# Kernel tuning notes

Measured on AMD Instinct MI355X. Metric: run time of the kernel, lower is better.

Reference implementation:

```python
import jax, jax.numpy as jnp
import numpy as np

N_HEADS = 16


def setup_inputs() -> dict:
    key = jax.random.key(0)
    ks = jax.random.split(key, 9)
    B, S, D = 4, 2048, 1024
    query = jax.random.normal(ks[0], (B, S, D), dtype=jnp.float32)
    key_t = jax.random.normal(ks[1], (B, S, D), dtype=jnp.float32)
    value = jax.random.normal(ks[2], (B, S, D), dtype=jnp.float32)
    mask = jax.random.randint(ks[3], (B, 1, S, S), 0, 10) > 0
    scale_w = 0.02  # keep exp(attention) in a safe range
    Wq = jax.random.normal(ks[4], (D, D), dtype=jnp.float32) * scale_w
    Wk = jax.random.normal(ks[5], (D, D), dtype=jnp.float32) * scale_w
    Wv = jax.random.normal(ks[6], (D, D), dtype=jnp.float32) * scale_w
    fc_w = jax.random.normal(ks[7], (D, D), dtype=jnp.float32) * scale_w
    fc_b = jnp.zeros((D,), dtype=jnp.float32)
    return {"query": query, "key": key_t, "value": value, "mask": mask,
            "Wq": Wq, "Wk": Wk, "Wv": Wv, "fc_w": fc_w, "fc_b": fc_b}


def reference(query, key, value, mask, Wq, Wk, Wv, fc_w, fc_b):
    B, S, D = query.shape
    H = N_HEADS
    Dh = D // H
    scale = jnp.sqrt(jnp.asarray(D / H, dtype=query.dtype))
    # Faithful to original: direct reshape [B,S,D] -> [B,H,S,Dh] (no transpose)
    Q = (query @ Wq.T).reshape(B, H, S, Dh)
    K = (key @ Wk.T).reshape(B, H, S, Dh)
    V = (value @ Wv.T).reshape(B, H, S, Dh)
    attn = jnp.einsum('bhqd,bhkd->bhqk', Q, K) / scale  # [B,H,S,S]
    # Hand-rolled masked softmax: exp, masked_fill(False->0), normalize, nan->0
    temp = jnp.where(mask, jnp.exp(attn), 0.0)
    attn = temp / jnp.sum(temp, axis=-1, keepdims=True)
    attn = jnp.where(jnp.isnan(attn), 0.0, attn)
    res = jnp.einsum('bhqk,bhkd->bhqd', attn, V)  # [B,H,S,Dh]
    outs = res.transpose(0, 2, 1, 3).reshape(B, S, D)
    outs = outs @ fc_w.T + fc_b
    return outs, res.transpose(1, 0, 2, 3)
```

## Files before the change

kernel.cpp:

```cpp
#include <hip/hip_runtime.h>


typedef __attribute__((ext_vector_type(8))) short bf16x8;
typedef __attribute__((ext_vector_type(4))) short bf16x4;
typedef __attribute__((ext_vector_type(4))) float f32x4;

#define MFMA32(a, b, c) __builtin_amdgcn_mfma_f32_16x16x32_bf16(a, b, c, 0, 0, 0)

#define GLDS16(g, l)                                                                       \
  __builtin_amdgcn_global_load_lds((const __attribute__((address_space(1))) void*)(g),     \
                                   (__attribute__((address_space(3))) void*)(l), 16, 0, 0)

static __device__ __forceinline__ float fast_exp2(float x) {
#if __has_builtin(__builtin_amdgcn_exp2f)
  return __builtin_amdgcn_exp2f(x);
#else
  return __expf(x * 0.69314718056f);
#endif
}

__device__ __forceinline__ unsigned short fbf(float f) {
  union { float f; unsigned u; } x; x.f = f;
  unsigned r = x.u + 0x7fffu + ((x.u >> 16) & 1u);
  return (unsigned short)(r >> 16);
}

static __device__ __forceinline__ bf16x4 pack2(unsigned lo, unsigned hi) {
  union { unsigned u[2]; bf16x4 v; } x; x.u[0] = lo; x.u[1] = hi; return x.v;
}

static __device__ __forceinline__ bf16x8 cat2(bf16x4 lo, bf16x4 hi) {
  union { bf16x4 h[2]; bf16x8 v; } x; x.h[0] = lo; x.h[1] = hi; return x.v;
}

static __device__ __forceinline__ bf16x4 epp(f32x4 s, unsigned pre, int sh) {
  union { float f; unsigned u; } e0, e1, e2, e3;
  e0.f = fast_exp2(s[0]); e1.f = fast_exp2(s[1]);
  e2.f = fast_exp2(s[2]); e3.f = fast_exp2(s[3]);
  unsigned p01 = __builtin_amdgcn_perm(e1.u + 0x8000u, e0.u + 0x8000u, 0x07060302u);
  unsigned p23 = __builtin_amdgcn_perm(e3.u + 0x8000u, e2.u + 0x8000u, 0x07060302u);
  int m0 = __builtin_amdgcn_sbfe(pre, sh + 0, 1), m1 = __builtin_amdgcn_sbfe(pre, sh + 1, 1);
  int m2 = __builtin_amdgcn_sbfe(pre, sh + 2, 1), m3 = __builtin_amdgcn_sbfe(pre, sh + 3, 1);
  unsigned k01 = __builtin_amdgcn_perm((unsigned)m1, (unsigned)m0, 0x07060100u);
  unsigned k23 = __builtin_amdgcn_perm((unsigned)m3, (unsigned)m2, 0x07060100u);
  return pack2(p01 & k01, p23 & k23);
}

__global__ __launch_bounds__(256) void prep_kernel(const float* __restrict__ s0,
                                                   const float* __restrict__ s1,
                                                   const float* __restrict__ s2,
                                                   const float* __restrict__ w0,
                                                   const float* __restrict__ w1,
                                                   const float* __restrict__ w2,
                                                   const float* __restrict__ w3,
                                                   unsigned short* __restrict__ d0,
                                                   unsigned short* __restrict__ d1,
                                                   unsigned short* __restrict__ d2,
                                                   unsigned short* __restrict__ e0,
                                                   unsigned short* __restrict__ e1,
                                                   unsigned short* __restrict__ e2,
                                                   unsigned short* __restrict__ e3) {
  int bid = blockIdx.x;
  const float* s;
  unsigned short* d;
  int i;
  if (bid < 24576) {
    int z = bid >> 13;
    s = (z == 0) ? s0 : (z == 1) ? s1 : s2;
    d = (z == 0) ? d0 : (z == 1) ? d1 : d2;
    i = (bid & 8191) * 256 + threadIdx.x;
  } else {
    int r = bid - 24576;
    int z = r >> 10;
    s = (z == 0) ? w0 : (z == 1) ? w1 : (z == 2) ? w2 : w3;
    d = (z == 0) ? e0 : (z == 1) ? e1 : (z == 2) ? e2 : e3;
    i = (r & 1023) * 256 + threadIdx.x;
  }
  float4 v = ((const float4*)s)[i];
  ushort4 o;
  o.x = fbf(v.x); o.y = fbf(v.y); o.z = fbf(v.z); o.w = fbf(v.w);
  ((ushort4*)d)[i] = o;
}

__global__ __launch_bounds__(256) void pack_mask_kernel(const int* __restrict__ m,
                                                        unsigned long long* __restrict__ o) {
  int i = blockIdx.x * 256 + threadIdx.x;
  unsigned long long b = __ballot(m[i] != 0);
  if ((threadIdx.x & 63) == 0) {
    int row = i >> 11;
    int kt = (i >> 7) & 15;
    int h = (i >> 6) & 1;
    o[(kt * 8192 + row) * 2 + h] = b;
  }
}

__global__ __launch_bounds__(256) void vtrans_kernel(const unsigned short* __restrict__ Vf,
                                                     unsigned short* __restrict__ Vt) {
  __shared__ unsigned short T[64][72];
  const int bh = blockIdx.y;
  const int s0 = blockIdx.x * 64;
  const int tid = threadIdx.x;
  {
    int r = tid >> 2, c = (tid & 3) * 16;
    const unsigned short* src = Vf + bh * 131072 + (s0 + r) * 64 + c;
    uint4 v0 = *(const uint4*)(src);
    uint4 v1 = *(const uint4*)(src + 8);
    *(uint4*)&T[r][c] = v0;
    *(uint4*)&T[r][c + 8] = v1;
  }
  __syncthreads();
  {
    int dh = tid & 63, rb = (tid >> 6) * 16;
    unsigned short o[16];
#pragma unroll
    for (int j = 0; j < 16; ++j) o[j] = T[rb + j][dh];
    unsigned short* dst = Vt + bh * 131072 + dh * 2048 + s0 + rb;
    *(uint4*)dst = *(const uint4*)&o[0];
    *(uint4*)(dst + 8) = *(const uint4*)&o[8];
  }
}

__global__ __launch_bounds__(256) void proj_kernel(const unsigned short* __restrict__ A0,
                                                   const unsigned short* __restrict__ A1,
                                                   const unsigned short* __restrict__ A2,
                                                   const unsigned short* __restrict__ W0,
                                                   const unsigned short* __restrict__ W1,
                                                   const unsigned short* __restrict__ W2,
                                                   unsigned short* __restrict__ C0,
                                                   unsigned short* __restrict__ C1,
                                                   unsigned short* __restrict__ C2) {
  __shared__ unsigned short Alds[128 * 64];
  __shared__ unsigned short Blds[128 * 64];
  const int flat = (blockIdx.z * 64 + blockIdx.y) * 8 + blockIdx.x;
  const int wid = (flat & 7) * 192 + (flat >> 3);
  const int z = wid >> 9;
  const int by = (wid >> 3) & 63;
  const int bx = wid & 7;
  const unsigned short* A = (z == 0) ? A0 : (z == 1) ? A1 : A2;
  const unsigned short* B = (z == 0) ? W0 : (z == 1) ? W1 : W2;
  const int tid = threadIdx.x;
  const int w = tid >> 6, l = tid & 63, q4 = l >> 4, c16 = l & 15;
  const int wm = w & 1, wn = w >> 1;
  const int mBase = by * 128, nBase = bx * 128;

  f32x4 acc[4][4];
#pragma unroll
  for (int a0 = 0; a0 < 4; ++a0)
#pragma unroll
    for (int a1 = 0; a1 < 4; ++a1) acc[a0][a1] = (f32x4){0.f, 0.f, 0.f, 0.f};

  const int rsub = tid >> 3;
  const int csw = ((tid & 7) ^ (rsub & 7)) * 8;

  for (int kt = 0; kt < 16; ++kt) {
    __syncthreads();
#pragma unroll
    for (int j = 0; j < 4; ++j) {
      const unsigned short* gA = A + (mBase + j * 32 + rsub) * 1024 + kt * 64 + csw;
      const unsigned short* gB = B + (nBase + j * 32 + rsub) * 1024 + kt * 64 + csw;
      GLDS16(gA, &Alds[(j * 256 + tid) * 8]);
      GLDS16(gB, &Blds[(j * 256 + tid) * 8]);
    }
    __syncthreads();

#pragma unroll
    for (int kk = 0; kk < 2; ++kk) {
      bf16x8 af[4], bfr[4];
#pragma unroll
      for (int mi = 0; mi < 4; ++mi) {
        int row = wm * 64 + mi * 16 + c16;
        af[mi] = *(const bf16x8*)&Alds[(row * 64 + ((q4 ^ (c16 & 7)) * 8)) ^ (kk << 5)];
      }
#pragma unroll
      for (int ni = 0; ni < 4; ++ni) {
        int row = wn * 64 + ni * 16 + c16;
        bfr[ni] = *(const bf16x8*)&Blds[(row * 64 + ((q4 ^ (c16 & 7)) * 8)) ^ (kk << 5)];
      }
#pragma unroll
      for (int mi = 0; mi < 4; ++mi)
#pragma unroll
        for (int ni = 0; ni < 4; ++ni) acc[mi][ni] = MFMA32(af[mi], bfr[ni], acc[mi][ni]);
    }
  }

  unsigned short* C = (z == 0) ? C0 : (z == 1) ? C1 : C2;
  const float scale = (z == 0) ? 0.18033688f : 1.0f;
#pragma unroll
  for (int mi = 0; mi < 4; ++mi) {
#pragma unroll
    for (int ni = 0; ni < 4; ++ni) {
#pragma unroll
      for (int rg = 0; rg < 4; ++rg) {
        int row = mBase + wm * 64 + mi * 16 + q4 * 4 + rg;
        int col = nBase + wn * 64 + ni * 16 + c16;
        C[row * 1024 + col] = fbf(acc[mi][ni][rg] * scale);
      }
    }
  }
}

__global__ __launch_bounds__(256) void gemm_out(const unsigned short* __restrict__ A,
                                                const unsigned short* __restrict__ B,
                                                float* __restrict__ C,
                                                const float* __restrict__ bias) {
  __shared__ unsigned short Alds[128 * 64];
  __shared__ unsigned short Blds[128 * 64];
  const int flat = blockIdx.y * 8 + blockIdx.x;
  const int wid = (flat & 7) * 64 + (flat >> 3);
  const int by = wid >> 3, bx = wid & 7;
  const int tid = threadIdx.x;
  const int w = tid >> 6, l = tid & 63, q4 = l >> 4, c16 = l & 15;
  const int wm = w & 1, wn = w >> 1;
  const int mBase = by * 128, nBase = bx * 128;

  f32x4 acc[4][4];
#pragma unroll
  for (int a0 = 0; a0 < 4; ++a0)
#pragma unroll
    for (int a1 = 0; a1 < 4; ++a1) acc[a0][a1] = (f32x4){0.f, 0.f, 0.f, 0.f};

  const int rsub = tid >> 3;
  const int csw = ((tid & 7) ^ (rsub & 7)) * 8;

  for (int kt = 0; kt < 16; ++kt) {
    __syncthreads();
#pragma unroll
    for (int j = 0; j < 4; ++j) {
      const unsigned short* gA = A + (mBase + j * 32 + rsub) * 1024 + kt * 64 + csw;
      const unsigned short* gB = B + (nBase + j * 32 + rsub) * 1024 + kt * 64 + csw;
      GLDS16(gA, &Alds[(j * 256 + tid) * 8]);
      GLDS16(gB, &Blds[(j * 256 + tid) * 8]);
    }
    __syncthreads();

#pragma unroll
    for (int kk = 0; kk < 2; ++kk) {
      bf16x8 af[4], bfr[4];
#pragma unroll
      for (int mi = 0; mi < 4; ++mi) {
        int row = wm * 64 + mi * 16 + c16;
        af[mi] = *(const bf16x8*)&Alds[(row * 64 + ((q4 ^ (c16 & 7)) * 8)) ^ (kk << 5)];
      }
#pragma unroll
      for (int ni = 0; ni < 4; ++ni) {
        int row = wn * 64 + ni * 16 + c16;
        bfr[ni] = *(const bf16x8*)&Blds[(row * 64 + ((q4 ^ (c16 & 7)) * 8)) ^ (kk << 5)];
      }
#pragma unroll
      for (int mi = 0; mi < 4; ++mi)
#pragma unroll
        for (int ni = 0; ni < 4; ++ni) acc[mi][ni] = MFMA32(af[mi], bfr[ni], acc[mi][ni]);
    }
  }

#pragma unroll
  for (int mi = 0; mi < 4; ++mi) {
#pragma unroll
    for (int ni = 0; ni < 4; ++ni) {
#pragma unroll
      for (int rg = 0; rg < 4; ++rg) {
        int row = mBase + wm * 64 + mi * 16 + q4 * 4 + rg;
        int col = nBase + wn * 64 + ni * 16 + c16;
        C[row * 1024 + col] = acc[mi][ni][rg] + bias[col];
      }
    }
  }
}

__global__ __launch_bounds__(256, 4) void flash_kernel(const unsigned short* __restrict__ Q,
                                                       const unsigned short* __restrict__ K,
                                                       const unsigned short* __restrict__ Vt,
                                                       const uint4* __restrict__ mb,
                                                       unsigned short* __restrict__ Cws,
                                                       float* __restrict__ res2) {
  __shared__ unsigned short Klds[128 * 64];
  __shared__ unsigned short Vtlds[64 * 128];
  const int tid = threadIdx.x;
  const int w = tid >> 6, l = tid & 63, q4 = l >> 4, c16 = l & 15;
  const int q44 = q4 * 4;
  const int flat = (blockIdx.z * 16 + blockIdx.y) * 16 + blockIdx.x;
  const int wid = (flat & 7) * 128 + (flat >> 3);
  const int qt = wid & 15, h = (wid >> 4) & 15, b = wid >> 8;
  const unsigned short* Qh = Q + (b * 2048 + h * 128) * 1024;
  const unsigned short* Kh = K + (b * 2048 + h * 128) * 1024;
  const unsigned short* Vth = Vt + (b * 16 + h) * 64 * 2048;

  bf16x8 qf[2][2];
#pragma unroll
  for (int i = 0; i < 2; ++i)
#pragma unroll
    for (int kc = 0; kc < 2; ++kc)
      qf[i][kc] = *(const bf16x8*)(Qh + (qt * 128 + w * 32 + i * 16 + c16) * 64 + kc * 32 + q4 * 8);

  const int rowi = b * 2048 + qt * 128 + w * 32 + c16;

  const int kOff = (tid >> 3) * 64 + (((tid & 7) ^ ((tid >> 3) & 7)) * 8);
  const int vOff = (tid >> 4) * 2048 + (((tid & 15) ^ (tid >> 4)) * 8);

  const int kb0 = c16 * 64 + ((q4 ^ (c16 & 7)) * 8);
  const int kb1 = kb0 ^ 32;
  const int vb = c16 * 128 + (q4 & 1) * 4;
  const int q41 = q4 >> 1;

  const bf16x8 ones8 = {(short)0x3F80, (short)0x3F80, (short)0x3F80, (short)0x3F80,
                        (short)0x3F80, (short)0x3F80, (short)0x3F80, (short)0x3F80};

  f32x4 oacc[2][4], soacc[2];
#pragma unroll
  for (int i = 0; i < 2; ++i) {
    soacc[i] = (f32x4){0.f, 0.f, 0.f, 0.f};
#pragma unroll
    for (int t = 0; t < 4; ++t) oacc[i][t] = (f32x4){0.f, 0.f, 0.f, 0.f};
  }

  for (int kt = 0; kt < 16; ++kt) {
    const unsigned short* gk = Kh + kt * 8192 + kOff;
    const unsigned short* gv = Vth + kt * 128 + vOff;
#pragma unroll
    for (int j = 0; j < 4; ++j) {
      GLDS16(gk + j * 2048, &Klds[(j * 256 + tid) * 8]);
      GLDS16(gv + j * 32768, &Vtlds[(j * 256 + tid) * 8]);
    }
    uint4 m0 = mb[kt * 8192 + rowi];
    uint4 m1 = mb[kt * 8192 + rowi + 16];
    unsigned pre0[4] = {m0.x >> q44, m0.y >> q44, m0.z >> q44, m0.w >> q44};
    unsigned pre1[4] = {m1.x >> q44, m1.y >> q44, m1.z >> q44, m1.w >> q44};
    __syncthreads();

#pragma unroll
    for (int m = 0; m < 4; ++m) {
      bf16x8 kfE0 = *(const bf16x8*)(Klds + kb0 + (2 * m) * 1024);
      bf16x8 kfE1 = *(const bf16x8*)(Klds + kb1 + (2 * m) * 1024);
      bf16x8 kfO0 = *(const bf16x8*)(Klds + kb0 + (2 * m + 1) * 1024);
      bf16x8 kfO1 = *(const bf16x8*)(Klds + kb1 + (2 * m + 1) * 1024);
      f32x4 sE0 = {0.f, 0.f, 0.f, 0.f}, sE1 = {0.f, 0.f, 0.f, 0.f};
      f32x4 sO0 = {0.f, 0.f, 0.f, 0.f}, sO1 = {0.f, 0.f, 0.f, 0.f};
      sE0 = MFMA32(kfE0, qf[0][0], sE0); sE0 = MFMA32(kfE1, qf[0][1], sE0);
      sE1 = MFMA32(kfE0, qf[1][0], sE1); sE1 = MFMA32(kfE1, qf[1][1], sE1);
      sO0 = MFMA32(kfO0, qf[0][0], sO0); sO0 = MFMA32(kfO1, qf[0][1], sO0);
      sO1 = MFMA32(kfO0, qf[1][0], sO1); sO1 = MFMA32(kfO1, qf[1][1], sO1);

      int shE = 0, shO = 16;
      bf16x8 pf0 = cat2(epp(sE0, pre0[m], shE), epp(sO0, pre0[m], shO));
      bf16x8 pf1 = cat2(epp(sE1, pre1[m], shE), epp(sO1, pre1[m], shO));

      int pLo = (4 * m + q41) ^ c16;
      int aLo = vb + pLo * 8;
#pragma unroll
      for (int t = 0; t < 4; ++t) {
        bf16x4 vlo = *(const bf16x4*)(Vtlds + aLo + t * 2048);
        bf16x4 vhi = *(const bf16x4*)(Vtlds + (aLo ^ 16) + t * 2048);
        bf16x8 vf8 = cat2(vlo, vhi);
        oacc[0][t] = MFMA32(vf8, pf0, oacc[0][t]);
        oacc[1][t] = MFMA32(vf8, pf1, oacc[1][t]);
      }
      soacc[0] = MFMA32(ones8, pf0, soacc[0]);
      soacc[1] = MFMA32(ones8, pf1, soacc[1]);
    }
    __syncthreads();
  }

#pragma unroll
  for (int i = 0; i < 2; ++i) {
    float sum = soacc[i][0];
    float rcp = (sum > 0.f) ? (1.0f / sum) : 0.f;
    int q = qt * 128 + w * 32 + i * 16 + c16;
    float* rp = res2 + (((h * 4 + b) * 2048 + q) * 64 + q44);
    unsigned short* cp = Cws + ((b * 2048 + q) * 1024 + h * 64 + q44);
#pragma unroll
    for (int t = 0; t < 4; ++t) {
      float o0 = oacc[i][t][0] * rcp, o1 = oacc[i][t][1] * rcp;
      float o2 = oacc[i][t][2] * rcp, o3 = oacc[i][t][3] * rcp;
      float4 fo = {o0, o1, o2, o3};
      *(float4*)(rp + t * 16) = fo;
      ushort4 cv = {fbf(o0), fbf(o1), fbf(o2), fbf(o3)};
      *(ushort4*)(cp + t * 16) = cv;
    }
  }
}

extern "C" void kernel_launch(void* const* d_in, const int* in_sizes, int n_in,
                              void* d_out, int out_size, void* d_ws, size_t ws_size,
                              hipStream_t stream) {
  const float* query = (const float*)d_in[0];
  const float* key_t = (const float*)d_in[1];
  const float* value = (const float*)d_in[2];
  const int* mask = (const int*)d_in[3];
  const float* Wq = (const float*)d_in[4];
  const float* Wk = (const float*)d_in[5];
  const float* Wv = (const float*)d_in[6];
  const float* fcw = (const float*)d_in[7];
  const float* fcb = (const float*)d_in[8];
  float* out = (float*)d_out;

  char* ws = (char*)d_ws;
  unsigned short* qbf = (unsigned short*)(ws);
  unsigned short* kbf = (unsigned short*)(ws + (16u << 20));
  unsigned short* vbf = (unsigned short*)(ws + (32u << 20));
  unsigned short* wqb = (unsigned short*)(ws + (48u << 20));
  unsigned short* wkb = (unsigned short*)(ws + (50u << 20));
  unsigned short* wvb = (unsigned short*)(ws + (52u << 20));
  unsigned short* fwb = (unsigned short*)(ws + (54u << 20));
  unsigned short* Qf = (unsigned short*)(ws + (56u << 20));
  unsigned short* Kf = (unsigned short*)(ws + (72u << 20));
  unsigned short* Vnat = (unsigned short*)(ws + (88u << 20));
  unsigned short* Cws = qbf;
  unsigned long long* mbits = (unsigned long long*)kbf;
  unsigned short* Vt = vbf;

  prep_kernel<<<28672, 256, 0, stream>>>(query, key_t, value, Wq, Wk, Wv, fcw,
                                         qbf, kbf, vbf, wqb, wkb, wvb, fwb);

  proj_kernel<<<dim3(8, 64, 3), 256, 0, stream>>>(qbf, kbf, vbf, wqb, wkb, wvb,
                                                  Qf, Kf, Vnat);

  vtrans_kernel<<<dim3(32, 64), 256, 0, stream>>>(Vnat, Vt);

  pack_mask_kernel<<<65536, 256, 0, stream>>>(mask, mbits);

  flash_kernel<<<dim3(16, 16, 4), 256, 0, stream>>>(Qf, Kf, Vt, (const uint4*)mbits, Cws,
                                                    out + 8388608);

  gemm_out<<<dim3(8, 64), 256, 0, stream>>>(Cws, fwb, out, fcb);
}
```

Measured before the change: 409.2 us.

## Double-buffer LDS tiles with prefetch in projection and output GEMMs

Both GEMM kernels now use two LDS buffers with K=32 tiles, prefetching the next tile via global_load_lds while computing MFMAs on the current one, with one barrier per step. This is meant to hide global load latency behind compute. It drops the XOR swizzle on the LDS layout, which risks bank conflicts on fragment reads, and halves the K depth per barrier.

```diff
diff --git a/kernel.cpp b/kernel.cpp
--- a/kernel.cpp
+++ b/kernel.cpp
@@ -129,8 +129,8 @@
                                                    unsigned short* __restrict__ C0,
                                                    unsigned short* __restrict__ C1,
                                                    unsigned short* __restrict__ C2) {
-  __shared__ unsigned short Alds[128 * 64];
-  __shared__ unsigned short Blds[128 * 64];
+  __shared__ unsigned short Al[2][128 * 32];
+  __shared__ unsigned short Bl[2][128 * 32];
   const int flat = (blockIdx.z * 64 + blockIdx.y) * 8 + blockIdx.x;
   const int wid = (flat & 7) * 192 + (flat >> 3);
   const int z = wid >> 9;
@@ -149,38 +149,40 @@
 #pragma unroll
     for (int a1 = 0; a1 < 4; ++a1) acc[a0][a1] = (f32x4){0.f, 0.f, 0.f, 0.f};
 
-  const int rsub = tid >> 3;
-  const int csw = ((tid & 7) ^ (rsub & 7)) * 8;
-
-  for (int kt = 0; kt < 16; ++kt) {
+  const int r0 = tid >> 2, cc0 = tid & 3;
+  const unsigned short* ga0 = A + (mBase + r0) * 1024 + cc0 * 8;
+  const unsigned short* ga1 = A + (mBase + 64 + r0) * 1024 + cc0 * 8;
+  const unsigned short* gb0 = B + (nBase + r0) * 1024 + cc0 * 8;
+  const unsigned short* gb1 = B + (nBase + 64 + r0) * 1024 + cc0 * 8;
+
+  GLDS16(ga0, &Al[0][tid * 8]);
+  GLDS16(ga1, &Al[0][(tid + 256) * 8]);
+  GLDS16(gb0, &Bl[0][tid * 8]);
+  GLDS16(gb1, &Bl[0][(tid + 256) * 8]);
+  __syncthreads();
+
+  int cur = 0;
+  for (int kt = 0; kt < 32; ++kt) {
+    if (kt < 31) {
+      int ko = (kt + 1) * 32;
+      GLDS16(ga0 + ko, &Al[cur ^ 1][tid * 8]);
+      GLDS16(ga1 + ko, &Al[cur ^ 1][(tid + 256) * 8]);
+      GLDS16(gb0 + ko, &Bl[cur ^ 1][tid * 8]);
+      GLDS16(gb1 + ko, &Bl[cur ^ 1][(tid + 256) * 8]);
+    }
+    bf16x8 af[4], bfr[4];
+#pragma unroll
+    for (int mi = 0; mi < 4; ++mi)
+      af[mi] = *(const bf16x8*)&Al[cur][(wm * 64 + mi * 16 + c16) * 32 + q4 * 8];
+#pragma unroll
+    for (int ni = 0; ni < 4; ++ni)
+      bfr[ni] = *(const bf16x8*)&Bl[cur][(wn * 64 + ni * 16 + c16) * 32 + q4 * 8];
+#pragma unroll
+    for (int mi = 0; mi < 4; ++mi)
+#pragma unroll
+      for (int ni = 0; ni < 4; ++ni) acc[mi][ni] = MFMA32(af[mi], bfr[ni], acc[mi][ni]);
     __syncthreads();
-#pragma unroll
-    for (int j = 0; j < 4; ++j) {
-      const unsigned short* gA = A + (mBase + j * 32 + rsub) * 1024 + kt * 64 + csw;
-      const unsigned short* gB = B + (nBase + j * 32 + rsub) * 1024 + kt * 64 + csw;
-      GLDS16(gA, &Alds[(j * 256 + tid) * 8]);
-      GLDS16(gB, &Blds[(j * 256 + tid) * 8]);
-    }
-    __syncthreads();
-
-#pragma unroll
-    for (int kk = 0; kk < 2; ++kk) {
-      bf16x8 af[4], bfr[4];
-#pragma unroll
-      for (int mi = 0; mi < 4; ++mi) {
-        int row = wm * 64 + mi * 16 + c16;
-        af[mi] = *(const bf16x8*)&Alds[(row * 64 + ((q4 ^ (c16 & 7)) * 8)) ^ (kk << 5)];
-      }
-#pragma unroll
-      for (int ni = 0; ni < 4; ++ni) {
-        int row = wn * 64 + ni * 16 + c16;
-        bfr[ni] = *(const bf16x8*)&Blds[(row * 64 + ((q4 ^ (c16 & 7)) * 8)) ^ (kk << 5)];
-      }
-#pragma unroll
-      for (int mi = 0; mi < 4; ++mi)
-#pragma unroll
-        for (int ni = 0; ni < 4; ++ni) acc[mi][ni] = MFMA32(af[mi], bfr[ni], acc[mi][ni]);
-    }
+    cur ^= 1;
   }
 
   unsigned short* C = (z == 0) ? C0 : (z == 1) ? C1 : C2;
@@ -203,8 +205,8 @@
                                                 const unsigned short* __restrict__ B,
                                                 float* __restrict__ C,
                                                 const float* __restrict__ bias) {
-  __shared__ unsigned short Alds[128 * 64];
-  __shared__ unsigned short Blds[128 * 64];
+  __shared__ unsigned short Al[2][128 * 32];
+  __shared__ unsigned short Bl[2][128 * 32];
   const int flat = blockIdx.y * 8 + blockIdx.x;
   const int wid = (flat & 7) * 64 + (flat >> 3);
   const int by = wid >> 3, bx = wid & 7;
@@ -219,38 +221,40 @@
 #pragma unroll
     for (int a1 = 0; a1 < 4; ++a1) acc[a0][a1] = (f32x4){0.f, 0.f, 0.f, 0.f};
 
-  const int rsub = tid >> 3;
-  const int csw = ((tid & 7) ^ (rsub & 7)) * 8;
-
-  for (int kt = 0; kt < 16; ++kt) {
+  const int r0 = tid >> 2, cc0 = tid & 3;
+  const unsigned short* ga0 = A + (mBase + r0) * 1024 + cc0 * 8;
+  const unsigned short* ga1 = A + (mBase + 64 + r0) * 1024 + cc0 * 8;
+  const unsigned short* gb0 = B + (nBase + r0) * 1024 + cc0 * 8;
+  const unsigned short* gb1 = B + (nBase + 64 + r0) * 1024 + cc0 * 8;
+
+  GLDS16(ga0, &Al[0][tid * 8]);
+  GLDS16(ga1, &Al[0][(tid + 256) * 8]);
+  GLDS16(gb0, &Bl[0][tid * 8]);
+  GLDS16(gb1, &Bl[0][(tid + 256) * 8]);
+  __syncthreads();
+
+  int cur = 0;
+  for (int kt = 0; kt < 32; ++kt) {
+    if (kt < 31) {
+      int ko = (kt + 1) * 32;
+      GLDS16(ga0 + ko, &Al[cur ^ 1][tid * 8]);
+      GLDS16(ga1 + ko, &Al[cur ^ 1][(tid + 256) * 8]);
+      GLDS16(gb0 + ko, &Bl[cur ^ 1][tid * 8]);
+      GLDS16(gb1 + ko, &Bl[cur ^ 1][(tid + 256) * 8]);
+    }
+    bf16x8 af[4], bfr[4];
+#pragma unroll
+    for (int mi = 0; mi < 4; ++mi)
+      af[mi] = *(const bf16x8*)&Al[cur][(wm * 64 + mi * 16 + c16) * 32 + q4 * 8];
+#pragma unroll
+    for (int ni = 0; ni < 4; ++ni)
+      bfr[ni] = *(const bf16x8*)&Bl[cur][(wn * 64 + ni * 16 + c16) * 32 + q4 * 8];
+#pragma unroll
+    for (int mi = 0; mi < 4; ++mi)
+#pragma unroll
+      for (int ni = 0; ni < 4; ++ni) acc[mi][ni] = MFMA32(af[mi], bfr[ni], acc[mi][ni]);
     __syncthreads();
-#pragma unroll
-    for (int j = 0; j < 4; ++j) {
-      const unsigned short* gA = A + (mBase + j * 32 + rsub) * 1024 + kt * 64 + csw;
-      const unsigned short* gB = B + (nBase + j * 32 + rsub) * 1024 + kt * 64 + csw;
-      GLDS16(gA, &Alds[(j * 256 + tid) * 8]);
-      GLDS16(gB, &Blds[(j * 256 + tid) * 8]);
-    }
-    __syncthreads();
-
-#pragma unroll
-    for (int kk = 0; kk < 2; ++kk) {
-      bf16x8 af[4], bfr[4];
-#pragma unroll
-      for (int mi = 0; mi < 4; ++mi) {
-        int row = wm * 64 + mi * 16 + c16;
-        af[mi] = *(const bf16x8*)&Alds[(row * 64 + ((q4 ^ (c16 & 7)) * 8)) ^ (kk << 5)];
-      }
-#pragma unroll
-      for (int ni = 0; ni < 4; ++ni) {
-        int row = wn * 64 + ni * 16 + c16;
-        bfr[ni] = *(const bf16x8*)&Blds[(row * 64 + ((q4 ^ (c16 & 7)) * 8)) ^ (kk << 5)];
-      }
-#pragma unroll
-      for (int mi = 0; mi < 4; ++mi)
-#pragma unroll
-        for (int ni = 0; ni < 4; ++ni) acc[mi][ni] = MFMA32(af[mi], bfr[ni], acc[mi][ni]);
-    }
+    cur ^= 1;
   }
 
 #pragma unroll
```

Result: slower. 423.6 us (+3.5%).
